# Kernel tuning notes

Measured on AMD Instinct MI355X. Metric: run time of the kernel, lower is better.

The kernel has to match this reference:

```python
import jax, jax.numpy as jnp
from jax import lax
import numpy as np

# pywt db5 decomposition low-pass filter
_DB5 = np.array([0.003335725285001549, -0.012580751999015526, -0.006241490213011705,
                 0.07757149384006515, -0.03224486958502952, -0.24229488706619015,
                 0.13842814590110342, 0.7243085284385744, 0.6038292697974729,
                 0.160102397974125], dtype=np.float32)
_L = 10       # filter length (db5)
_LEVELS = 5   # decomp_level
_NT = 15      # SURE tuning grid size


def _filters():
    dec_lo = jnp.asarray(_DB5)
    sign = jnp.asarray(((-1.0) ** (np.arange(_L) + 1)).astype(np.float32))
    dec_hi = sign * dec_lo[::-1]          # QMF: g[k] = (-1)^(k+1) h[L-1-k]
    return dec_lo, dec_hi, dec_lo[::-1], dec_hi[::-1]


def _dwt1d(x, dlo, dhi):
    # x: (B, N) -> (B, 2, floor((N+L-1)/2)); pywt 'symmetric' convention
    p = _L - 1
    xe = jnp.pad(x, ((0, 0), (p, p)), mode='symmetric')[:, 1:]
    k = jnp.stack([dlo[::-1], dhi[::-1]])[:, None, :]  # (2,1,L), true convolution
    return lax.conv_general_dilated(xe[:, None, :], k, (2,), 'VALID',
                                    dimension_numbers=('NCH', 'OIH', 'NCH'))


def _idwt1d(a, d, rlo, rhi, n_out):
    # a,d: (B, M) -> (B, n_out); zero-upsample via lhs_dilation, full conv, crop L-2
    k = jnp.stack([rlo[::-1], rhi[::-1]])[None, :, :]  # (1,2,L)
    y = lax.conv_general_dilated(jnp.stack([a, d], axis=1), k, (1,),
                                 [(_L - 1, _L - 1)], lhs_dilation=(2,),
                                 dimension_numbers=('NCH', 'OIH', 'NCH'))
    return y[:, 0, _L - 2:_L - 2 + n_out]


def _dwt2_level(x, dlo, dhi):
    # x: (C, H, W) -> ll (C,Hd,Wd), highs (C,3,Hd,Wd)
    C, H, W = x.shape
    yw = _dwt1d(x.reshape(C * H, W), dlo, dhi).reshape(C, H, 2, -1)
    Wd = yw.shape[-1]
    yw = yw.transpose(0, 2, 3, 1)  # (C, wband, Wd, H)
    yh = _dwt1d(yw.reshape(C * 2 * Wd, H), dlo, dhi).reshape(C, 2, Wd, 2, -1)
    yh = yh.transpose(0, 1, 3, 4, 2)  # (C, wband, hband, Hd, Wd)
    ll = yh[:, 0, 0]
    highs = jnp.stack([yh[:, 0, 1], yh[:, 1, 0], yh[:, 1, 1]], axis=1)
    return ll, highs


def _idwt2_level(ll, highs, rlo, rhi, h_out, w_out):
    C, Hd, Wd = ll.shape
    lh, hl, hh = highs[:, 0], highs[:, 1], highs[:, 2]

    def inv_h(a, d):  # inverse along H axis
        at = a.transpose(0, 2, 1).reshape(C * Wd, Hd)
        dt = d.transpose(0, 2, 1).reshape(C * Wd, Hd)
        r = _idwt1d(at, dt, rlo, rhi, h_out)
        return r.reshape(C, Wd, h_out).transpose(0, 2, 1)

    lo_w = inv_h(ll, lh)
    hi_w = inv_h(hl, hh)
    r = _idwt1d(lo_w.reshape(C * h_out, Wd), hi_w.reshape(C * h_out, Wd),
                rlo, rhi, w_out)
    return r.reshape(C, h_out, w_out)


def _est_additive_noise(data):
    eps = 1e-6
    C = data.shape[0]
    ddp = data @ data.T
    ddpi = jnp.linalg.inv(ddp + eps * jnp.eye(C, dtype=data.dtype))

    def per_band(i):
        xx = ddpi - jnp.outer(ddpi[:, i], ddpi[i, :]) / ddpi[i, i]
        ddpa = ddp[:, i].at[i].set(0.0)
        beta = (xx @ ddpa).at[i].set(0.0)
        return data[i] - beta @ data

    return jax.vmap(per_band)(jnp.arange(C))


def _hyres(x, min_iter):
    dlo, dhi, rlo, rhi = _filters()
    H, W, C = x.shape
    N = H * W
    # 1) noise estimation -> per-band noise power omega1
    w = _est_additive_noise(x.reshape(N, C).T)               # (C, N)
    omega1 = (jnp.sqrt(jnp.var(w, axis=1, ddof=1)) + 1e-30) ** 2  # (C,)
    y_w = x * omega1 ** -0.5
    # 2) PCA: y_w2d = (U*S) @ Vh ; pc = scores as image cube
    u, s, vh = jnp.linalg.svd(y_w.reshape(N, C), full_matrices=False)
    pc = (u * s).reshape(H, W, C).transpose(2, 0, 1)         # (C, H, W)
    # 3) multi-level 2D DWT per band
    xmax, xmin = x.max(), x.min()
    ll = pc
    highs, sizes = [], []
    for _ in range(_LEVELS):
        sizes.append(ll.shape[1:])
        ll, hi = _dwt2_level(ll, dlo, dhi)
        highs.append(hi)
    ll = jnp.nan_to_num(ll, nan=0.0, posinf=xmax, neginf=xmin)
    highs = [jnp.nan_to_num(h, nan=0.0, posinf=xmax, neginf=xmin) for h in highs]
    # 4) flatten all coefficients -> (M, C)
    flat = [ll.reshape(C, -1)] + [h.reshape(C, -1) for h in highs]
    vperm = jnp.concatenate(flat, axis=1).T
    M = vperm.shape[0]
    norm2 = jnp.sum(vperm * vperm)
    K = norm2 - float(M * C)
    # 5) per-band SURE over a fixed threshold grid (vectorized over bands)
    x2 = vperm ** 2
    t_max = float(np.sqrt(np.log(M)))
    t_grid = jnp.linspace(0.0, t_max, _NT)

    def sure_at(t):
        t2 = t * t
        cnt = jnp.sum(x2 >= t2, axis=0).astype(vperm.dtype)
        sm = jnp.sum(jnp.minimum(x2, t2), axis=0)
        return sm + 2.0 * cnt - float(M)

    sure_all = jax.vmap(sure_at)(t_grid)                     # (NT, C)
    # 6) cumulative SURE recurrence S_r = sum_{j<r} S_j + a_r + K ; min over grid

    def step(cum, a_r):
        s_r = cum + a_r + K
        return cum + s_r, jnp.min(s_r)

    _, min_sure = lax.scan(step, jnp.zeros(_NT, vperm.dtype), sure_all.T)
    prev = jnp.concatenate([min_sure[:1], min_sure[:-1]])
    idx = jnp.arange(C)
    cond = (idx > min_iter) & jnp.logical_not(min_sure > 2.0 * prev)
    rank = jnp.where(jnp.any(cond), jnp.argmax(cond), C - 1)
    # 7) keep bands < rank (zeroing == slicing since iDWT/matmul are per-band linear)
    keep = (idx < rank).astype(vperm.dtype)
    ll_k = ll * keep[:, None, None]
    highs_k = [h * keep[:, None, None, None] for h in highs]
    y_est = ll_k
    for hi, (h_out, w_out) in zip(reversed(highs_k), reversed(sizes)):
        y_est = _idwt2_level(y_est, hi, rlo, rhi, h_out, w_out)
    y2d = y_est.transpose(1, 2, 0).reshape(N, C)
    y_restored = ((omega1 ** 0.5) * (y2d @ vh).reshape(H, W, C))
    return y_restored


def setup_inputs() -> dict:
    key = jax.random.key(0)
    x = jax.random.uniform(key, (256, 256, 191), dtype=jnp.float32)
    return {"x": x, "min_iter": 2}


def reference(x, min_iter):
    return _hyres(x, min_iter)
```

## Files before the change

kernel.cpp:

```cpp
#include <hip/hip_runtime.h>
#include <math.h>
#include <cstdint>

#define CH 191
#define NPIX 65536
#define MCOEF 74287
#define CSTRIDE 74288
#define SW32 4
#define NSKEW (96 * 194)

__device__ const float g_dlo[10] = {
  0.003335725285001549f, -0.012580751999015526f, -0.006241490213011705f,
  0.07757149384006515f, -0.03224486958502952f, -0.24229488706619015f,
  0.13842814590110342f, 0.7243085284385744f, 0.6038292697974729f,
  0.160102397974125f };
__device__ const float g_dhi[10] = {
  -0.160102397974125f, 0.6038292697974729f, -0.7243085284385744f,
  0.13842814590110342f, 0.24229488706619015f, -0.03224486958502952f,
  -0.07757149384006515f, -0.006241490213011705f, 0.012580751999015526f,
  0.003335725285001549f };

struct TArgs { double t2[15]; };

__device__ __forceinline__ int sk(int a, int b) {
  int s = a + b; if (s >= CH) s -= CH;
  int d = a - b; if (d < 0) d = -d;
  int df = (d > 95) ? (CH - d) : d;
  return df * 194 + s;
}

#define BAR_LGKM() asm volatile("s_waitcnt lgkmcnt(0)\n\ts_barrier" ::: "memory")

__global__ __launch_bounds__(256) void k_ddp(const float* __restrict__ x,
                                             double* __restrict__ ddp) {
  __shared__ float as[32][33];
  __shared__ float bs[32][33];
  int i0 = blockIdx.x * 32, j0 = blockIdx.y * 32;
  if (j0 < i0) return;
  int t = threadIdx.x;
  int n0 = blockIdx.z * 4096;
  int tx = t & 15, ty = t >> 4;
  double a00 = 0, a01 = 0, a10 = 0, a11 = 0;
  for (int nb = 0; nb < 4096; nb += 32) {
    for (int e = t; e < 1024; e += 256) {
      int kk = e >> 5, ii = e & 31;
      int n = n0 + nb + kk;
      as[kk][ii] = (i0 + ii < CH) ? x[(size_t)n * CH + i0 + ii] : 0.f;
      bs[kk][ii] = (j0 + ii < CH) ? x[(size_t)n * CH + j0 + ii] : 0.f;
    }
    __syncthreads();
    #pragma unroll 8
    for (int kk = 0; kk < 32; ++kk) {
      double x0 = as[kk][tx], x1 = as[kk][tx + 16];
      double y0 = bs[kk][ty], y1 = bs[kk][ty + 16];
      a00 += x0 * y0; a01 += x0 * y1; a10 += x1 * y0; a11 += x1 * y1;
    }
    __syncthreads();
  }
  int i = i0 + tx, j = j0 + ty;
  if (i < CH) {
    if (j < CH)      atomicAdd(&ddp[i * CH + j], a00);
    if (j + 16 < CH) atomicAdd(&ddp[i * CH + j + 16], a01);
  }
  if (i + 16 < CH) {
    if (j < CH)      atomicAdd(&ddp[(i + 16) * CH + j], a10);
    if (j + 16 < CH) atomicAdd(&ddp[(i + 16) * CH + j + 16], a11);
  }
}

__global__ void k_mirror(double* __restrict__ ddp) {
  int e = blockIdx.x * 256 + threadIdx.x;
  if (e >= CH * CH) return;
  int i = e / CH, j = e % CH;
  if (i > j) ddp[e] = ddp[j * CH + i];
}

__global__ __launch_bounds__(256) void k_rsum(const float* __restrict__ x,
                                              double* __restrict__ rsum) {
  int t = threadIdx.x;
  if (t >= CH) return;
  int row0 = blockIdx.x * 256;
  double a = 0;
  for (int r = 0; r < 256; ++r) a += (double)x[(size_t)(row0 + r) * CH + t];
  atomicAdd(&rsum[t], a);
}

__global__ __launch_bounds__(768) void k_gj(const double* __restrict__ ddp,
                                            float* __restrict__ out) {
  __shared__ float fc[192];
  int t = threadIdx.x;
  int i = t % 192;
  int cg = t / 192;
  int j0 = cg * 48;
  bool act = (i < CH);
  float a[48];
  #pragma unroll
  for (int m = 0; m < 48; ++m) {
    int j = j0 + m;
    a[m] = (act && j < CH) ? (float)(ddp[i * CH + j] + ((i == j) ? 1e-6 : 0.0)) : 0.f;
  }
  if (t < 192) fc[t] = 0.f;
  __syncthreads();
  for (int k = 0; k < CH; ++k) {
    int cgk = k / 48;
    int mk = k - cgk * 48;
    if (cg == cgk && act) {
      float v = 0.f;
      #pragma unroll
      for (int m = 0; m < 48; ++m) v = (m == mk) ? a[m] : v;
      fc[i] = v;
    }
    __syncthreads();
    float dinv = 1.0f / fc[k];
    float fci = fc[i];
    bool iskrow = (i == k);
    float s = fci * dinv;
    float colv = iskrow ? (-dinv) : s;
    #pragma unroll
    for (int mq = 0; mq < 12; ++mq) {
      float4 f4 = *(const float4*)&fc[j0 + mq * 4];
      #pragma unroll
      for (int c4 = 0; c4 < 4; ++c4) {
        int m = mq * 4 + c4;
        float fj = (c4 == 0) ? f4.x : (c4 == 1) ? f4.y : (c4 == 2) ? f4.z : f4.w;
        float gen = iskrow ? (fj * dinv) : (a[m] - s * fj);
        bool iskcol = (cg == cgk) && (m == mk);
        a[m] = iskcol ? colv : gen;
      }
    }
    __syncthreads();
  }
  if (act) {
    #pragma unroll
    for (int m = 0; m < 48; ++m) {
      int j = j0 + m;
      if (j < CH) out[i * CH + j] = -a[m];
    }
  }
}

__global__ void k_newton1(const double* __restrict__ ddp, const float* __restrict__ X,
                          double* __restrict__ T) {
  int j = blockIdx.x * 16 + threadIdx.x, i = blockIdx.y * 16 + threadIdx.y;
  if (i >= CH || j >= CH) return;
  double acc = 0;
  for (int k = 0; k < CH; ++k) {
    double a = ddp[i * CH + k] + (i == k ? 1e-6 : 0.0);
    acc += a * (double)X[k * CH + j];
  }
  T[i * CH + j] = (i == j ? 2.0 : 0.0) - acc;
}
__global__ void k_newton2(const float* __restrict__ X, const double* __restrict__ T,
                          double* __restrict__ P) {
  int j = blockIdx.x * 16 + threadIdx.x, i = blockIdx.y * 16 + threadIdx.y;
  if (i >= CH || j >= CH) return;
  double acc = 0;
  for (int k = 0; k < CH; ++k) acc += (double)X[i * CH + k] * T[k * CH + j];
  P[i * CH + j] = acc;
}

__global__ __launch_bounds__(256) void k_beta(const double* __restrict__ ddp,
                                              const double* __restrict__ P,
                                              const double* __restrict__ rsum,
                                              double* __restrict__ sqrtom,
                                              double* __restrict__ invs) {
  __shared__ double bet[CH];
  __shared__ double red[256];
  int i = blockIdx.x, t = threadIdx.x;
  double pii = P[i * CH + i];
  for (int j = t; j < CH; j += 256) {
    double pjip = P[j * CH + i] / pii;
    double acc = 0;
    for (int k = 0; k < CH; ++k) {
      double ddpa = (k == i) ? 0.0 : ddp[k * CH + i];
      acc += (P[j * CH + k] - pjip * P[i * CH + k]) * ddpa;
    }
    bet[j] = (j == i) ? 0.0 : acc;
  }
  __syncthreads();
  double s1 = 0, s2 = 0;
  for (int j = t; j < CH; j += 256) {
    double gj = ((j == i) ? 1.0 : 0.0) - bet[j];
    s1 += gj * rsum[j];
    double tj = 0;
    for (int k = 0; k < CH; ++k) {
      double gk = ((k == i) ? 1.0 : 0.0) - bet[k];
      tj += ddp[j * CH + k] * gk;
    }
    s2 += gj * tj;
  }
  red[t] = s1; __syncthreads();
  for (int o = 128; o; o >>= 1) { if (t < o) red[t] += red[t + o]; __syncthreads(); }
  double sumw = red[0]; __syncthreads();
  red[t] = s2; __syncthreads();
  for (int o = 128; o; o >>= 1) { if (t < o) red[t] += red[t + o]; __syncthreads(); }
  if (t == 0) {
    double sumsq = red[0];
    double var = (sumsq - sumw * sumw / 65536.0) / 65535.0;
    if (var < 0) var = 0;
    double so = sqrt(var) + 1e-30;
    sqrtom[i] = so;
    invs[i] = 1.0 / so;
  }
}

__global__ void k_packG(const double* __restrict__ ddp, const double* __restrict__ invs,
                        float* __restrict__ Gsk, float* __restrict__ dgf,
                        double* __restrict__ G64) {
  int e = blockIdx.x * 256 + threadIdx.x;
  if (e >= CH * CH) return;
  int i = e / CH, j = e % CH;
  double v = ddp[e] * invs[i] * invs[j];
  G64[e] = v;
  if (j >= i) Gsk[sk(i, j)] = (float)v;
  if (j == i) dgf[i] = (float)v;
}

__global__ __launch_bounds__(1024) void k_jac32(const float* __restrict__ Gsk,
                                                const float* __restrict__ dg0,
                                                float2* __restrict__ rlogA) {
  extern __shared__ float As[];
  __shared__ float2 csn[96];
  __shared__ float dg[CH];
  int t = threadIdx.x;

  int jS[5], kS[5]; int ntask = 0;
  for (int id = t; id < 4560; id += 1024) {
    int j = 0, off = 0;
    while (off + (95 - j) <= id) { off += 95 - j; ++j; }
    jS[ntask] = j; kS[ntask] = j + 1 + (id - off);
    ++ntask;
  }
  int a00[5], a01[5], a10[5], a11[5], limA[5], limB[5];
  #pragma unroll
  for (int ii = 0; ii < 5; ++ii) {
    if (ii < ntask) {
      int j = jS[ii], k = kS[ii];
      int A = j + k;
      int B = k - j;
      int dfB = (A > 95) ? (CH - A) : A;
      int bA = B * 194;
      int bB = dfB * 194;
      a00[ii] = (bA + A) * 4;
      a11[ii] = (bA + CH - A) * 4;
      a01[ii] = (bB + CH - B) * 4;
      a10[ii] = (bB + B) * 4;
      limA[ii] = (bA + CH) * 4;
      limB[ii] = (bB + CH) * 4;
    } else {
      a00[ii] = a01[ii] = a10[ii] = a11[ii] = 0;
      limA[ii] = limB[ii] = 1 << 30; jS[ii] = 0; kS[ii] = 1;
    }
  }

  for (int e = t; e < NSKEW; e += 1024) As[e] = Gsk[e];
  if (t < CH) dg[t] = dg0[t];
  __syncthreads();

  const char* Asb = (const char*)As;
  for (int sweep = 0; sweep < SW32; ++sweep) {
    for (int r = 0; r < CH; ++r) {
      float m0[5], m1[5], m2[5], m3[5];
      #pragma unroll
      for (int ii = 0; ii < 5; ++ii) {
        if (ii < ntask) {
          m0[ii] = *(const float*)(Asb + a00[ii]);
          m1[ii] = *(const float*)(Asb + a01[ii]);
          if (jS[ii] != 0) {
            m2[ii] = *(const float*)(Asb + a10[ii]);
            m3[ii] = *(const float*)(Asb + a11[ii]);
          }
        }
      }
      if (t >= 1 && t < 96) {
        int p = r + t; if (p >= CH) p -= CH;
        int q = r - t; if (q < 0) q += CH;
        int ipq = sk(p, q);
        float app = dg[p], aqq = dg[q], apq = As[ipq];
        float c = 1.0f, s = 0.0f, piv = apq, dp = app, dq = aqq;
        if (fabsf(apq) > 3e-7f * (fabsf(app) + fabsf(aqq)) + 1e-30f) {
          float tau = (aqq - app) / (2.0f * apq);
          float tt = copysignf(1.0f, tau) / (fabsf(tau) + sqrtf(1.0f + tau * tau));
          c = 1.0f / sqrtf(1.0f + tt * tt); s = tt * c;
          dp = app - tt * apq; dq = aqq + tt * apq; piv = 0.0f;
        }
        dg[p] = dp; dg[q] = dq;
        As[ipq] = piv;
        csn[t] = make_float2(c, s);
        rlogA[((size_t)(sweep * CH + r)) * 95 + (t - 1)] = make_float2(c, s);
      }
      BAR_LGKM();
      #pragma unroll
      for (int ii = 0; ii < 5; ++ii) {
        if (ii < ntask) {
          float2 ck2 = csn[kS[ii]];
          if (jS[ii] == 0) {
            float vp = m0[ii], vq = m1[ii];
            *(float*)((char*)As + a00[ii]) = ck2.x * vp - ck2.y * vq;
            *(float*)((char*)As + a01[ii]) = ck2.y * vp + ck2.x * vq;
          } else {
            float2 cj2 = csn[jS[ii]];
            float n00 = ck2.x * m0[ii] - ck2.y * m1[ii];
            float n01 = ck2.y * m0[ii] + ck2.x * m1[ii];
            float n10 = ck2.x * m2[ii] - ck2.y * m3[ii];
            float n11 = ck2.y * m2[ii] + ck2.x * m3[ii];
            *(float*)((char*)As + a00[ii]) = cj2.x * n00 - cj2.y * n10;
            *(float*)((char*)As + a10[ii]) = cj2.y * n00 + cj2.x * n10;
            *(float*)((char*)As + a01[ii]) = cj2.x * n01 - cj2.y * n11;
            *(float*)((char*)As + a11[ii]) = cj2.y * n01 + cj2.x * n11;
          }
          a00[ii] += 8; if (a00[ii] >= limA[ii]) a00[ii] -= 764;
          a11[ii] += 8; if (a11[ii] >= limA[ii]) a11[ii] -= 764;
          a01[ii] += 8; if (a01[ii] >= limB[ii]) a01[ii] -= 764;
          a10[ii] += 8; if (a10[ii] >= limB[ii]) a10[ii] -= 764;
        }
      }
      BAR_LGKM();
    }
  }
}

__global__ __launch_bounds__(128) void k_replayA(const float2* __restrict__ rlogA,
                                                 double* __restrict__ Q) {
  __shared__ double vr[CH];
  int row = blockIdx.x, t = threadIdx.x;
  const int NR = SW32 * CH;
  for (int j = t; j < CH; j += 128) vr[j] = (j == row) ? 1.0 : 0.0;
  bool act = (t < 95);
  float2 nb[4];
  #pragma unroll
  for (int u = 0; u < 4; ++u)
    nb[u] = (act && u < NR) ? rlogA[(size_t)u * 95 + t] : make_float2(1.f, 0.f);
  BAR_LGKM();
  int r = 0;
  for (int g = 0; g < NR; g += 4) {
    #pragma unroll
    for (int u = 0; u < 4; ++u) {
      float2 cur = nb[u];
      int gn = g + u + 4;
      nb[u] = (act && gn < NR) ? rlogA[(size_t)gn * 95 + t] : make_float2(1.f, 0.f);
      if (act && cur.y != 0.f) {
        int k = t + 1;
        int p = r + k; if (p >= CH) p -= CH;
        int q = r - k; if (q < 0) q += CH;
        double s = (double)cur.y;
        double c = sqrt(fmax(0.0, 1.0 - s * s));
        double vp = vr[p], vq = vr[q];
        vr[p] = c * vp - s * vq;
        vr[q] = s * vp + c * vq;
      }
      if (++r == CH) r = 0;
      BAR_LGKM();
    }
  }
  for (int j = t; j < CH; j += 128) Q[(size_t)row * CH + j] = vr[j];
}

__global__ void k_gq(const double* __restrict__ G64, const double* __restrict__ Q,
                     double* __restrict__ T) {
  int j = blockIdx.x * 16 + threadIdx.x, i = blockIdx.y * 16 + threadIdx.y;
  if (i >= CH || j >= CH) return;
  double acc = 0;
  for (int k = 0; k < CH; ++k) acc += G64[i * CH + k] * Q[(size_t)k * CH + j];
  T[i * CH + j] = acc;
}
__global__ void k_qtq(const double* __restrict__ Q, const double* __restrict__ T,
                      double* __restrict__ A2sk, double* __restrict__ dg64) {
  int j = blockIdx.x * 16 + threadIdx.x, i = blockIdx.y * 16 + threadIdx.y;
  if (i >= CH || j >= CH || j < i) return;
  double acc = 0;
  for (int k = 0; k < CH; ++k) acc += Q[(size_t)k * CH + i] * T[k * CH + j];
  if (j == i) dg64[i] = acc;
  else A2sk[sk(i, j)] = acc;
}

__global__ __launch_bounds__(1024) void k_jac64(const double* __restrict__ A2sk,
                                                const double* __restrict__ dg0,
                                                double* __restrict__ eig,
                                                double2* __restrict__ rlogB) {
  extern __shared__ double As64[];
  __shared__ double2 csn[96];
  __shared__ double dg[CH];
  int t = threadIdx.x;

  int jS[5], kS[5]; int ntask = 0;
  for (int id = t; id < 4560; id += 1024) {
    int j = 0, off = 0;
    while (off + (95 - j) <= id) { off += 95 - j; ++j; }
    jS[ntask] = j; kS[ntask] = j + 1 + (id - off);
    ++ntask;
  }
  int a00[5], a01[5], a10[5], a11[5], limA[5], limB[5];
  #pragma unroll
  for (int ii = 0; ii < 5; ++ii) {
    if (ii < ntask) {
      int j = jS[ii], k = kS[ii];
      int A = j + k;
      int B = k - j;
      int dfB = (A > 95) ? (CH - A) : A;
      int bA = B * 194;
      int bB = dfB * 194;
      a00[ii] = (bA + A) * 8;
      a11[ii] = (bA + CH - A) * 8;
      a01[ii] = (bB + CH - B) * 8;
      a10[ii] = (bB + B) * 8;
      limA[ii] = (bA + CH) * 8;
      limB[ii] = (bB + CH) * 8;
    } else {
      a00[ii] = a01[ii] = a10[ii] = a11[ii] = 0;
      limA[ii] = limB[ii] = 1 << 30; jS[ii] = 0; kS[ii] = 1;
    }
  }

  for (int e = t; e < NSKEW; e += 1024) As64[e] = A2sk[e];
  if (t < CH) dg[t] = dg0[t];
  __syncthreads();

  const char* Asb = (const char*)As64;
  for (int r = 0; r < CH; ++r) {
    double m0[5], m1[5], m2[5], m3[5];
    #pragma unroll
    for (int ii = 0; ii < 5; ++ii) {
      if (ii < ntask) {
        m0[ii] = *(const double*)(Asb + a00[ii]);
        m1[ii] = *(const double*)(Asb + a01[ii]);
        if (jS[ii] != 0) {
          m2[ii] = *(const double*)(Asb + a10[ii]);
          m3[ii] = *(const double*)(Asb + a11[ii]);
        }
      }
    }
    if (t >= 1 && t < 96) {
      int p = r + t; if (p >= CH) p -= CH;
      int q = r - t; if (q < 0) q += CH;
      int ipq = sk(p, q);
      double app = dg[p], aqq = dg[q], apq = As64[ipq];
      double c = 1.0, s = 0.0, piv = apq, dp = app, dq = aqq;
      if (fabs(apq) > 4e-16 * (fabs(app) + fabs(aqq)) + 1e-300) {
        double tau = (aqq - app) / (2.0 * apq);
        double tt = copysign(1.0, tau) / (fabs(tau) + sqrt(1.0 + tau * tau));
        c = 1.0 / sqrt(1.0 + tt * tt); s = tt * c;
        dp = app - tt * apq; dq = aqq + tt * apq; piv = 0.0;
      }
      dg[p] = dp; dg[q] = dq;
      As64[ipq] = piv;
      csn[t] = make_double2(c, s);
      rlogB[(size_t)r * 95 + (t - 1)] = make_double2(c, s);
    }
    BAR_LGKM();
    #pragma unroll
    for (int ii = 0; ii < 5; ++ii) {
      if (ii < ntask) {
        double2 ck2 = csn[kS[ii]];
        if (jS[ii] == 0) {
          double vp = m0[ii], vq = m1[ii];
          *(double*)((char*)As64 + a00[ii]) = ck2.x * vp - ck2.y * vq;
          *(double*)((char*)As64 + a01[ii]) = ck2.y * vp + ck2.x * vq;
        } else {
          double2 cj2 = csn[jS[ii]];
          double n00 = ck2.x * m0[ii] - ck2.y * m1[ii];
          double n01 = ck2.y * m0[ii] + ck2.x * m1[ii];
          double n10 = ck2.x * m2[ii] - ck2.y * m3[ii];
          double n11 = ck2.y * m2[ii] + ck2.x * m3[ii];
          *(double*)((char*)As64 + a00[ii]) = cj2.x * n00 - cj2.y * n10;
          *(double*)((char*)As64 + a10[ii]) = cj2.y * n00 + cj2.x * n10;
          *(double*)((char*)As64 + a01[ii]) = cj2.x * n01 - cj2.y * n11;
          *(double*)((char*)As64 + a11[ii]) = cj2.y * n01 + cj2.x * n11;
        }
        a00[ii] += 16; if (a00[ii] >= limA[ii]) a00[ii] -= 1528;
        a11[ii] += 16; if (a11[ii] >= limA[ii]) a11[ii] -= 1528;
        a01[ii] += 16; if (a01[ii] >= limB[ii]) a01[ii] -= 1528;
        a10[ii] += 16; if (a10[ii] >= limB[ii]) a10[ii] -= 1528;
      }
    }
    BAR_LGKM();
  }
  for (int i = t; i < CH; i += 1024) eig[i] = dg[i];
}

__global__ __launch_bounds__(128) void k_replayB(const double2* __restrict__ rlogB,
                                                 const double* __restrict__ Q,
                                                 double* __restrict__ V) {
  __shared__ double vr[CH];
  int row = blockIdx.x, t = threadIdx.x;
  const int NR = CH;
  for (int j = t; j < CH; j += 128) vr[j] = Q[(size_t)row * CH + j];
  double2 nxt = (t < 95) ? rlogB[t] : make_double2(1.0, 0.0);
  BAR_LGKM();
  for (int g = 0; g < NR; ++g) {
    double2 cur = nxt;
    if (t < 95 && g + 1 < NR) nxt = rlogB[(size_t)(g + 1) * 95 + t];
    if (t < 95 && cur.y != 0.0) {
      int k = t + 1;
      int p = g + k; if (p >= CH) p -= CH;
      int q = g - k; if (q < 0) q += CH;
      double vp = vr[p], vq = vr[q];
      vr[p] = cur.x * vp - cur.y * vq;
      vr[q] = cur.y * vp + cur.x * vq;
    }
    BAR_LGKM();
  }
  for (int j = t; j < CH; j += 128) V[(size_t)row * CH + j] = vr[j];
}

__global__ __launch_bounds__(256) void k_sortprep(const double* __restrict__ eig,
                                                  const double* __restrict__ V,
                                                  const double* __restrict__ invs,
                                                  int* __restrict__ perm,
                                                  float* __restrict__ Vw) {
  __shared__ double ev[CH];
  __shared__ int pm[CH];
  int t = threadIdx.x;
  if (t < CH) ev[t] = eig[t];
  __syncthreads();
  if (t < CH) {
    double my = ev[t];
    int rk = 0;
    for (int j = 0; j < CH; ++j) {
      double o = ev[j];
      rk += (o > my || (o == my && j < t)) ? 1 : 0;
    }
    pm[rk] = t;
  }
  __syncthreads();
  if (t < CH) perm[t] = pm[t];
  for (int e = t; e < 192 * 192; e += 256) {
    int k = e / 192, i = e - k * 192;
    float v = 0.f;
    if (k < CH && i < CH) v = (float)(invs[k] * V[(size_t)k * CH + pm[i]]);
    Vw[e] = v;
  }
}

__global__ __launch_bounds__(256) void k_pc(const float* __restrict__ x,
                                            const float* __restrict__ Vw,
                                            float* __restrict__ pcT) {
  __shared__ float xs[16][65];
  __shared__ float vs[16][33];
  int n0 = blockIdx.x * 64, i0 = blockIdx.y * 32;
  int t = threadIdx.x;
  int tn = t & 15, ti = t >> 4;
  float acc[4][2] = {};
  for (int k0 = 0; k0 < 192; k0 += 16) {
    {
      int col = t & 15, row = t >> 4;
      #pragma unroll
      for (int rr = 0; rr < 4; ++rr) {
        int nn = row + rr * 16;
        int k = k0 + col;
        xs[col][nn] = (k < CH) ? x[(size_t)(n0 + nn) * CH + k] : 0.f;
      }
    }
    {
      int ii = t & 31, kk = t >> 5;
      vs[kk][ii] = Vw[(k0 + kk) * 192 + i0 + ii];
      vs[kk + 8][ii] = Vw[(k0 + kk + 8) * 192 + i0 + ii];
    }
    __syncthreads();
    #pragma unroll
    for (int kk = 0; kk < 16; ++kk) {
      float b0 = vs[kk][ti], b1 = vs[kk][ti + 16];
      #pragma unroll
      for (int rr = 0; rr < 4; ++rr) {
        float a = xs[kk][tn + rr * 16];
        acc[rr][0] += a * b0;
        acc[rr][1] += a * b1;
      }
    }
    __syncthreads();
  }
  #pragma unroll
  for (int rr = 0; rr < 4; ++rr)
    #pragma unroll
    for (int bb = 0; bb < 2; ++bb) {
      int i = i0 + ti + bb * 16, n = n0 + tn + rr * 16;
      if (i < CH) pcT[(size_t)i * NPIX + n] = acc[rr][bb];
    }
}

__global__ __launch_bounds__(256) void k_row(const float* __restrict__ in,
                                             float* __restrict__ rb,
                                             int h, int w, int wd, int chS) {
  __shared__ float rowv[256];
  int bid = blockIdx.x;
  int c = bid / h, y = bid % h;
  const float* src = in + (size_t)c * chS + (size_t)y * w;
  int t = threadIdx.x;
  if (t < w) rowv[t] = src[t];
  __syncthreads();
  float* dst = rb + (size_t)(c * h + y) * (2 * wd);
  for (int o = t; o < 2 * wd; o += 256) {
    int b = (o >= wd) ? 1 : 0;
    int xp = b ? o - wd : o;
    float acc = 0.f;
    #pragma unroll
    for (int s = 0; s < 10; ++s) {
      int m = 2 * xp + 1 - s;
      if (m < 0) m = -1 - m;
      else if (m >= w) m = 2 * w - 1 - m;
      acc += (b ? g_dhi[s] : g_dlo[s]) * rowv[m];
    }
    dst[o] = acc;
  }
}

__global__ __launch_bounds__(256) void k_col(const float* __restrict__ rb,
                                             float* __restrict__ llout,
                                             float* __restrict__ coeff,
                                             int h, int wd, int hd, int chSout,
                                             int offHi, int offLL, int lastlvl) {
  int c = blockIdx.z, yp = blockIdx.y;
  int xq = blockIdx.x * 256 + threadIdx.x;
  if (xq >= 2 * wd) return;
  const float* base = rb + (size_t)c * h * 2 * wd + xq;
  float lo = 0.f, hi = 0.f;
  #pragma unroll
  for (int s = 0; s < 10; ++s) {
    int m = 2 * yp + 1 - s;
    if (m < 0) m = -1 - m;
    else if (m >= h) m = 2 * h - 1 - m;
    float v = base[(size_t)m * 2 * wd];
    lo += g_dlo[s] * v;
    hi += g_dhi[s] * v;
  }
  float* cc = coeff + (size_t)c * CSTRIDE;
  if (xq < wd) {
    llout[(size_t)c * chSout + (size_t)yp * wd + xq] = lo;
    if (lastlvl) cc[offLL + yp * wd + xq] = lo;
    cc[offHi + 0 * hd * wd + yp * wd + xq] = hi;
  } else {
    int xp = xq - wd;
    cc[offHi + 1 * hd * wd + yp * wd + xp] = lo;
    cc[offHi + 2 * hd * wd + yp * wd + xp] = hi;
  }
}

#define DWT_SMEM ((17424 + 18480) * 4)
__global__ __launch_bounds__(256) void k_dwt_tail(const float* __restrict__ llin,
                                                  float* __restrict__ coeff) {
  extern __shared__ float smem[];
  float* A = smem;
  float* B = smem + 17424;
  const int hsz[5]   = {132, 70, 39, 24, 16};
  const int offHiC[4] = {52272, 66972, 71535, 73263};
  int c = blockIdx.x, t = threadIdx.x;
  float* cc = coeff + (size_t)c * CSTRIDE;
  for (int e = t; e < 132 * 132; e += 256) A[e] = llin[(size_t)c * 17424 + e];
  BAR_LGKM();
  #pragma unroll
  for (int l = 0; l < 4; ++l) {
    const int h = hsz[l], w = hsz[l], wd = hsz[l + 1], hd = hsz[l + 1];
    const int w2 = 2 * wd;
    for (int e = t; e < h * w2; e += 256) {
      int y = e / w2, o = e - y * w2;
      int b = (o >= wd) ? 1 : 0;
      int xp = b ? o - wd : o;
      float acc = 0.f;
      #pragma unroll
      for (int s = 0; s < 10; ++s) {
        int m = 2 * xp + 1 - s;
        if (m < 0) m = -1 - m;
        else if (m >= w) m = 2 * w - 1 - m;
        acc += (b ? g_dhi[s] : g_dlo[s]) * A[y * w + m];
      }
      B[y * w2 + o] = acc;
    }
    BAR_LGKM();
    for (int e = t; e < hd * w2; e += 256) {
      int yp = e / w2, xq = e - yp * w2;
      float lo = 0.f, hi = 0.f;
      #pragma unroll
      for (int s = 0; s < 10; ++s) {
        int m = 2 * yp + 1 - s;
        if (m < 0) m = -1 - m;
        else if (m >= h) m = 2 * h - 1 - m;
        float v = B[m * w2 + xq];
        lo += g_dlo[s] * v;
        hi += g_dhi[s] * v;
      }
      if (xq < wd) {
        A[yp * wd + xq] = lo;
        if (l == 3) cc[74031 + yp * wd + xq] = lo;
        cc[offHiC[l] + 0 * hd * wd + yp * wd + xq] = hi;
      } else {
        int xp = xq - wd;
        cc[offHiC[l] + 1 * hd * wd + yp * wd + xp] = lo;
        cc[offHiC[l] + 2 * hd * wd + yp * wd + xp] = hi;
      }
    }
    BAR_LGKM();
  }
}

__global__ __launch_bounds__(256) void k_stats(const float* __restrict__ coeff,
                                               double* __restrict__ stats, TArgs ta) {
  int c = blockIdx.y;
  const float* cc = coeff + (size_t)c * CSTRIDE;
  double sm[15], cnt[15], nrm = 0;
  #pragma unroll
  for (int q = 0; q < 15; ++q) { sm[q] = 0; cnt[q] = 0; }
  for (int idx = blockIdx.x * 256 + threadIdx.x; idx < MCOEF; idx += 24 * 256) {
    double v = (double)cc[idx];
    double v2 = v * v;
    nrm += v2;
    #pragma unroll
    for (int q = 0; q < 15; ++q) {
      sm[q] += fmin(v2, ta.t2[q]);
      cnt[q] += (v2 >= ta.t2[q]) ? 1.0 : 0.0;
    }
  }
  __shared__ double wred[4][31];
  int lane = threadIdx.x & 63, wv = threadIdx.x >> 6;
  for (int q = 0; q < 31; ++q) {
    double val = (q < 15) ? sm[q] : ((q < 30) ? cnt[q - 15] : nrm);
    #pragma unroll
    for (int o = 32; o > 0; o >>= 1) val += __shfl_down(val, o);
    if (lane == 0) wred[wv][q] = val;
  }
  __syncthreads();
  if (threadIdx.x < 31) {
    double sum = wred[0][threadIdx.x] + wred[1][threadIdx.x] +
                 wred[2][threadIdx.x] + wred[3][threadIdx.x];
    atomicAdd(&stats[c * 31 + threadIdx.x], sum);
  }
}

__global__ __launch_bounds__(256) void k_sure(const double* __restrict__ stats,
                                              const double* __restrict__ sqrtom,
                                              const double* __restrict__ V,
                                              const int* __restrict__ perm,
                                              const int* __restrict__ min_iter_p,
                                              float* __restrict__ Wm,
                                              int* __restrict__ meta) {
  __shared__ double st[CH * 31];
  __shared__ double minsure[CH];
  __shared__ int rankS;
  int t = threadIdx.x;
  for (int e = t; e < CH * 31; e += 256) st[e] = stats[e];
  __syncthreads();
  if (t == 0) {
    double norm2 = 0;
    for (int c = 0; c < CH; ++c) norm2 += st[c * 31 + 30];
    double K = norm2 - (double)MCOEF * (double)CH;
    double cum[15];
    for (int q = 0; q < 15; ++q) cum[q] = 0;
    for (int r = 0; r < CH; ++r) {
      double mn = 1e300;
      for (int q = 0; q < 15; ++q) {
        double sure = st[r * 31 + q] + 2.0 * st[r * 31 + 15 + q] - (double)MCOEF;
        double s = cum[q] + sure + K;
        cum[q] += s;
        if (s < mn) mn = s;
      }
      minsure[r] = mn;
    }
    int mi = *min_iter_p;
    int rank = CH - 1;
    for (int r = 0; r < CH; ++r) {
      double prev = (r == 0) ? minsure[0] : minsure[r - 1];
      bool cond = (r > mi) && !(minsure[r] > 2.0 * prev);
      if (cond) { rank = r; break; }
    }
    rankS = rank;
    meta[1] = rank;
  }
  __syncthreads();
  int rank = rankS;
  for (int e = t; e < 192 * 192; e += 256) {
    int k = e / 192, c = e - k * 192;
    float v = 0.f;
    if (k < rank && c < CH) v = (float)(sqrtom[c] * V[(size_t)c * CH + perm[k]]);
    Wm[e] = v;
  }
}

__global__ __launch_bounds__(256) void k_out(const float* __restrict__ pcT,
                                             const float* __restrict__ Wm,
                                             float* __restrict__ out) {
  __shared__ float psx[16][65];
  __shared__ float wsx[16][33];
  int n0 = blockIdx.x * 64, c0 = blockIdx.y * 32;
  int t = threadIdx.x;
  int tc = t & 15, tn = t >> 4;
  float acc[4][2] = {};
  for (int k0 = 0; k0 < 192; k0 += 16) {
    {
      int nn = t & 63, kk0 = t >> 6;
      #pragma unroll
      for (int rr = 0; rr < 4; ++rr) {
        int kk = kk0 + rr * 4;
        int k = k0 + kk;
        psx[kk][nn] = (k < CH) ? pcT[(size_t)k * NPIX + n0 + nn] : 0.f;
      }
    }
    {
      int cc = t & 31, kk = t >> 5;
      wsx[kk][cc] = Wm[(k0 + kk) * 192 + c0 + cc];
      wsx[kk + 8][cc] = Wm[(k0 + kk + 8) * 192 + c0 + cc];
    }
    __syncthreads();
    #pragma unroll
    for (int kk = 0; kk < 16; ++kk) {
      float b0 = wsx[kk][tc], b1 = wsx[kk][tc + 16];
      #pragma unroll
      for (int rr = 0; rr < 4; ++rr) {
        float a = psx[kk][tn + rr * 16];
        acc[rr][0] += a * b0;
        acc[rr][1] += a * b1;
      }
    }
    __syncthreads();
  }
  #pragma unroll
  for (int rr = 0; rr < 4; ++rr)
    #pragma unroll
    for (int bb = 0; bb < 2; ++bb) {
      int n = n0 + tn + rr * 16, c = c0 + tc + bb * 16;
      if (c < CH) out[(size_t)n * CH + c] = acc[rr][bb];
    }
}

extern "C" void kernel_launch(void* const* d_in, const int* in_sizes, int n_in,
                              void* d_out, int out_size, void* d_ws, size_t ws_size,
                              hipStream_t stream) {
  const float* x = (const float*)d_in[0];
  const int* p_min_iter = (const int*)d_in[1];
  float* out = (float*)d_out;
  char* ws = (char*)d_ws;

  size_t cur = 0;
  auto A = [&](size_t b) { size_t o = cur; cur += (b + 511) & ~(size_t)511; return o; };
  double* ddp     = (double*)(ws + A((size_t)CH * CH * 8));
  double* ddpi64  = (double*)(ws + A((size_t)CH * CH * 8));
  double* Tm      = (double*)(ws + A((size_t)CH * CH * 8));
  double* V       = (double*)(ws + A((size_t)CH * CH * 8));
  double* G64     = (double*)(ws + A((size_t)CH * CH * 8));
  double* T64     = (double*)(ws + A((size_t)CH * CH * 8));
  double* Q       = (double*)(ws + A((size_t)CH * CH * 8));
  double* A2sk    = (double*)(ws + A((size_t)NSKEW * 8));
  double* dg64    = (double*)(ws + A((size_t)CH * 8));
  double* eig     = (double*)(ws + A((size_t)CH * 8));
  double* rsum    = (double*)(ws + A((size_t)CH * 8));
  double* sqrtom  = (double*)(ws + A((size_t)CH * 8));
  double* invs    = (double*)(ws + A((size_t)CH * 8));
  double* stats   = (double*)(ws + A((size_t)CH * 31 * 8));
  int* perm       = (int*)(ws + A((size_t)CH * 4));
  int* meta       = (int*)(ws + A(64));
  float* ddpi32   = (float*)(ws + A((size_t)CH * CH * 4));
  float* Gsk      = (float*)(ws + A((size_t)NSKEW * 4));
  float* dgf      = (float*)(ws + A((size_t)CH * 4));
  float* Vw       = (float*)(ws + A((size_t)192 * 192 * 4));
  float* Wm       = (float*)(ws + A((size_t)192 * 192 * 4));
  float2* rlogA   = (float2*)(ws + A((size_t)SW32 * CH * 95 * 8));
  double2* rlogB  = (double2*)(ws + A((size_t)CH * 95 * 16));
  float* pcT      = (float*)(ws + A((size_t)CH * NPIX * 4));
  float* rowbuf   = (float*)(ws + A((size_t)CH * 256 * 264 * 4));
  float* llA      = (float*)(ws + A((size_t)CH * 17424 * 4));
  float* coeff    = (float*)(ws + A((size_t)CH * CSTRIDE * 4));
  (void)ws_size; (void)in_sizes; (void)n_in; (void)out_size;

  hipMemsetAsync(ddp, 0, (size_t)CH * CH * 8, stream);
  hipMemsetAsync(rsum, 0, (size_t)CH * 8, stream);
  hipMemsetAsync(stats, 0, (size_t)CH * 31 * 8, stream);

  const int J32_SMEM = NSKEW * 4;
  const int J64_SMEM = NSKEW * 8;

  k_ddp<<<dim3(6, 6, 16), 256, 0, stream>>>(x, ddp);
  k_mirror<<<143, 256, 0, stream>>>(ddp);
  k_rsum<<<256, 256, 0, stream>>>(x, rsum);
  k_gj<<<1, 768, 0, stream>>>(ddp, ddpi32);
  k_newton1<<<dim3(12, 12), dim3(16, 16), 0, stream>>>(ddp, ddpi32, Tm);
  k_newton2<<<dim3(12, 12), dim3(16, 16), 0, stream>>>(ddpi32, Tm, ddpi64);
  k_beta<<<CH, 256, 0, stream>>>(ddp, ddpi64, rsum, sqrtom, invs);
  k_packG<<<143, 256, 0, stream>>>(ddp, invs, Gsk, dgf, G64);
  (void)hipFuncSetAttribute((const void*)k_jac32,
        hipFuncAttributeMaxDynamicSharedMemorySize, J32_SMEM);
  k_jac32<<<1, 1024, J32_SMEM, stream>>>(Gsk, dgf, rlogA);
  k_replayA<<<CH, 128, 0, stream>>>(rlogA, Q);
  k_gq<<<dim3(12, 12), dim3(16, 16), 0, stream>>>(G64, Q, T64);
  k_qtq<<<dim3(12, 12), dim3(16, 16), 0, stream>>>(Q, T64, A2sk, dg64);
  (void)hipFuncSetAttribute((const void*)k_jac64,
        hipFuncAttributeMaxDynamicSharedMemorySize, J64_SMEM);
  k_jac64<<<1, 1024, J64_SMEM, stream>>>(A2sk, dg64, eig, rlogB);
  k_replayB<<<CH, 128, 0, stream>>>(rlogB, Q, V);
  k_sortprep<<<1, 256, 0, stream>>>(eig, V, invs, perm, Vw);
  k_pc<<<dim3(1024, 6), 256, 0, stream>>>(x, Vw, pcT);

  k_row<<<CH * 256, 256, 0, stream>>>(pcT, rowbuf, 256, 256, 132, NPIX);
  k_col<<<dim3(2, 132, CH), 256, 0, stream>>>(
      rowbuf, llA, coeff, 256, 132, 132, 132 * 132, 0, 74031, 0);
  (void)hipFuncSetAttribute((const void*)k_dwt_tail,
        hipFuncAttributeMaxDynamicSharedMemorySize, DWT_SMEM);
  k_dwt_tail<<<CH, 256, DWT_SMEM, stream>>>(llA, coeff);

  TArgs ta;
  {
    double tmax = sqrt(log((double)MCOEF));
    for (int j = 0; j < 15; ++j) { double tv = tmax * j / 14.0; ta.t2[j] = tv * tv; }
  }
  k_stats<<<dim3(24, CH), 256, 0, stream>>>(coeff, stats, ta);
  k_sure<<<1, 256, 0, stream>>>(stats, sqrtom, V, perm, p_min_iter, Wm, meta);
  k_out<<<dim3(1024, 6), 256, 0, stream>>>(pcT, Wm, out);
}
```

Baseline: 3.670 ms.

## Widen pc/out GEMM tiles to 64x64 and streamline Gauss-Jordan pivot selection

The two projection GEMMs (k_pc, k_out) now use 64-wide channel tiles with a 4x4 per-thread register block instead of 32-wide tiles with 4x2. This halves the grid along the channel axis and raises arithmetic intensity per shared-memory load, so the pixel tile is fetched from global memory half as often. The single-block Gauss-Jordan inverse picks the pivot with a two-level select tree instead of a 48-way select chain, and the pivot-column fix-up moves out of the inner update loop. The trade-off is more registers per thread and fewer blocks in the GEMMs, which could lower occupancy.

Measured after the change: 4.368 ms. 19.0% more time.

```diff
diff --git a/kernel.cpp b/kernel.cpp
--- a/kernel.cpp
+++ b/kernel.cpp
@@ -105,9 +105,19 @@
     int cgk = k / 48;
     int mk = k - cgk * 48;
     if (cg == cgk && act) {
-      float v = 0.f;
-      #pragma unroll
-      for (int m = 0; m < 48; ++m) v = (m == mk) ? a[m] : v;
+      float g[12];
+      #pragma unroll
+      for (int gq = 0; gq < 12; ++gq) {
+        float v = a[gq * 4];
+        v = (mk == gq * 4 + 1) ? a[gq * 4 + 1] : v;
+        v = (mk == gq * 4 + 2) ? a[gq * 4 + 2] : v;
+        v = (mk == gq * 4 + 3) ? a[gq * 4 + 3] : v;
+        g[gq] = v;
+      }
+      int mq4 = mk >> 2;
+      float v = g[0];
+      #pragma unroll
+      for (int gq = 1; gq < 12; ++gq) v = (mq4 == gq) ? g[gq] : v;
       fc[i] = v;
     }
     __syncthreads();
@@ -115,7 +125,6 @@
     float fci = fc[i];
     bool iskrow = (i == k);
     float s = fci * dinv;
-    float colv = iskrow ? (-dinv) : s;
     #pragma unroll
     for (int mq = 0; mq < 12; ++mq) {
       float4 f4 = *(const float4*)&fc[j0 + mq * 4];
@@ -123,10 +132,13 @@
       for (int c4 = 0; c4 < 4; ++c4) {
         int m = mq * 4 + c4;
         float fj = (c4 == 0) ? f4.x : (c4 == 1) ? f4.y : (c4 == 2) ? f4.z : f4.w;
-        float gen = iskrow ? (fj * dinv) : (a[m] - s * fj);
-        bool iskcol = (cg == cgk) && (m == mk);
-        a[m] = iskcol ? colv : gen;
-      }
+        a[m] = iskrow ? (fj * dinv) : (a[m] - s * fj);
+      }
+    }
+    if (cg == cgk) {
+      float colv = iskrow ? (-dinv) : s;
+      #pragma unroll
+      for (int m = 0; m < 48; ++m) a[m] = (m == mk) ? colv : a[m];
     }
     __syncthreads();
   }
@@ -536,11 +548,11 @@
                                             const float* __restrict__ Vw,
                                             float* __restrict__ pcT) {
   __shared__ float xs[16][65];
-  __shared__ float vs[16][33];
-  int n0 = blockIdx.x * 64, i0 = blockIdx.y * 32;
+  __shared__ float vs[16][65];
+  int n0 = blockIdx.x * 64, i0 = blockIdx.y * 64;
   int t = threadIdx.x;
   int tn = t & 15, ti = t >> 4;
-  float acc[4][2] = {};
+  float acc[4][4] = {};
   for (int k0 = 0; k0 < 192; k0 += 16) {
     {
       int col = t & 15, row = t >> 4;
@@ -552,19 +564,23 @@
       }
     }
     {
-      int ii = t & 31, kk = t >> 5;
-      vs[kk][ii] = Vw[(k0 + kk) * 192 + i0 + ii];
-      vs[kk + 8][ii] = Vw[(k0 + kk + 8) * 192 + i0 + ii];
+      int ii = t & 63, kk = t >> 6;
+      #pragma unroll
+      for (int rr = 0; rr < 4; ++rr)
+        vs[kk + rr * 4][ii] = Vw[(k0 + kk + rr * 4) * 192 + i0 + ii];
     }
     __syncthreads();
     #pragma unroll
     for (int kk = 0; kk < 16; ++kk) {
       float b0 = vs[kk][ti], b1 = vs[kk][ti + 16];
+      float b2 = vs[kk][ti + 32], b3 = vs[kk][ti + 48];
       #pragma unroll
       for (int rr = 0; rr < 4; ++rr) {
         float a = xs[kk][tn + rr * 16];
         acc[rr][0] += a * b0;
         acc[rr][1] += a * b1;
+        acc[rr][2] += a * b2;
+        acc[rr][3] += a * b3;
       }
     }
     __syncthreads();
@@ -572,7 +588,7 @@
   #pragma unroll
   for (int rr = 0; rr < 4; ++rr)
     #pragma unroll
-    for (int bb = 0; bb < 2; ++bb) {
+    for (int bb = 0; bb < 4; ++bb) {
       int i = i0 + ti + bb * 16, n = n0 + tn + rr * 16;
       if (i < CH) pcT[(size_t)i * NPIX + n] = acc[rr][bb];
     }
@@ -778,11 +794,11 @@
                                              const float* __restrict__ Wm,
                                              float* __restrict__ out) {
   __shared__ float psx[16][65];
-  __shared__ float wsx[16][33];
-  int n0 = blockIdx.x * 64, c0 = blockIdx.y * 32;
+  __shared__ float wsx[16][65];
+  int n0 = blockIdx.x * 64, c0 = blockIdx.y * 64;
   int t = threadIdx.x;
   int tc = t & 15, tn = t >> 4;
-  float acc[4][2] = {};
+  float acc[4][4] = {};
   for (int k0 = 0; k0 < 192; k0 += 16) {
     {
       int nn = t & 63, kk0 = t >> 6;
@@ -794,19 +810,23 @@
       }
     }
     {
-      int cc = t & 31, kk = t >> 5;
-      wsx[kk][cc] = Wm[(k0 + kk) * 192 + c0 + cc];
-      wsx[kk + 8][cc] = Wm[(k0 + kk + 8) * 192 + c0 + cc];
+      int cc = t & 63, kk = t >> 6;
+      #pragma unroll
+      for (int rr = 0; rr < 4; ++rr)
+        wsx[kk + rr * 4][cc] = Wm[(k0 + kk + rr * 4) * 192 + c0 + cc];
     }
     __syncthreads();
     #pragma unroll
     for (int kk = 0; kk < 16; ++kk) {
       float b0 = wsx[kk][tc], b1 = wsx[kk][tc + 16];
+      float b2 = wsx[kk][tc + 32], b3 = wsx[kk][tc + 48];
       #pragma unroll
       for (int rr = 0; rr < 4; ++rr) {
         float a = psx[kk][tn + rr * 16];
         acc[rr][0] += a * b0;
         acc[rr][1] += a * b1;
+        acc[rr][2] += a * b2;
+        acc[rr][3] += a * b3;
       }
     }
     __syncthreads();
@@ -814,7 +834,7 @@
   #pragma unroll
   for (int rr = 0; rr < 4; ++rr)
     #pragma unroll
-    for (int bb = 0; bb < 2; ++bb) {
+    for (int bb = 0; bb < 4; ++bb) {
       int n = n0 + tn + rr * 16, c = c0 + tc + bb * 16;
       if (c < CH) out[(size_t)n * CH + c] = acc[rr][bb];
     }
@@ -885,7 +905,7 @@
   k_jac64<<<1, 1024, J64_SMEM, stream>>>(A2sk, dg64, eig, rlogB);
   k_replayB<<<CH, 128, 0, stream>>>(rlogB, Q, V);
   k_sortprep<<<1, 256, 0, stream>>>(eig, V, invs, perm, Vw);
-  k_pc<<<dim3(1024, 6), 256, 0, stream>>>(x, Vw, pcT);
+  k_pc<<<dim3(1024, 3), 256, 0, stream>>>(x, Vw, pcT);
 
   k_row<<<CH * 256, 256, 0, stream>>>(pcT, rowbuf, 256, 256, 132, NPIX);
   k_col<<<dim3(2, 132, CH), 256, 0, stream>>>(
@@ -901,5 +921,5 @@
   }
   k_stats<<<dim3(24, CH), 256, 0, stream>>>(coeff, stats, ta);
   k_sure<<<1, 256, 0, stream>>>(stats, sqrtom, V, perm, p_min_iter, Wm, meta);
-  k_out<<<dim3(1024, 6), 256, 0, stream>>>(pcT, Wm, out);
-}
+  k_out<<<dim3(1024, 3), 256, 0, stream>>>(pcT, Wm, out);
+}
```
